# Kernel tuning notes

Hardware: AMD Instinct MI355X
Metric: run time of the kernel (lower is better)

Reference implementation:

```python
import jax, jax.numpy as jnp
import numpy as np

N_DETS = 50000
DEG = 32
N_EDGES = N_DETS * DEG

def _xavier(key, fan_in, fan_out):
    lim = np.sqrt(6.0 / (fan_in + fan_out)).astype(np.float32)
    return jax.random.uniform(key, (fan_in, fan_out), jnp.float32, -lim, lim)

def setup_inputs() -> dict:
    key = jax.random.key(0)
    ks = jax.random.split(key, 10)
    detFeatures = jax.random.normal(ks[0], (N_DETS, 128), jnp.float32)
    # every detection has exactly DEG neighbor pairs -> sorted segment ids, no empty segments
    cIdxs = jnp.repeat(jnp.arange(N_DETS, dtype=jnp.int64), DEG)
    nIdxs = jax.random.randint(ks[1], (N_EDGES,), 0, N_DETS, jnp.int64)
    pairFeatures = jax.random.normal(ks[2], (N_EDGES, 32), jnp.float32)
    return {
        "detFeatures": detFeatures,
        "cIdxs": cIdxs,
        "nIdxs": nIdxs,
        "pairFeatures": pairFeatures,
        "W_fc1": _xavier(ks[3], 128, 32), "b_fc1": jnp.zeros((32,), jnp.float32),
        "W_pw1": _xavier(ks[4], 96, 64), "b_pw1": jnp.zeros((64,), jnp.float32),
        "W_pw2": _xavier(ks[5], 64, 64), "b_pw2": jnp.zeros((64,), jnp.float32),
        "W_pm1": _xavier(ks[6], 64, 64), "b_pm1": jnp.zeros((64,), jnp.float32),
        "W_pm2": _xavier(ks[7], 64, 64), "b_pm2": jnp.zeros((64,), jnp.float32),
        "W_out": _xavier(ks[8], 64, 128), "b_out": jnp.zeros((128,), jnp.float32),
    }

def reference(detFeatures, cIdxs, nIdxs, pairFeatures,
              W_fc1, b_fc1, W_pw1, b_pw1, W_pw2, b_pw2,
              W_pm1, b_pm1, W_pm2, b_pm2, W_out, b_out):
    relu = jax.nn.relu
    # fc1: [N,128] -> [N,32]
    h = relu(detFeatures @ W_fc1 + b_fc1)
    # gather center / neighbor feats per pair; zero neighbor feats on identity rows
    cFeats = h[cIdxs]                                   # [E,32]
    nFeats = jnp.where((cIdxs == nIdxs)[:, None], 0.0, h[nIdxs])  # [E,32]
    x = jnp.concatenate((pairFeatures, cFeats, nFeats), axis=1)   # [E,96]
    x = relu(x @ W_pw1 + b_pw1)                         # [E,64]
    x = relu(x @ W_pw2 + b_pw2)                         # [E,64]
    # per-detection segment max (replaces the O(N) python loop)
    m = jax.ops.segment_max(x, cIdxs, num_segments=detFeatures.shape[0])  # [N,64]
    m = relu(m @ W_pm1 + b_pm1)
    m = relu(m @ W_pm2 + b_pm2)
    refined = m @ W_out + b_out                         # [N,128]
    return relu(detFeatures + refined)
```

## Files before the change

kernel.cpp:

```cpp
#include <hip/hip_runtime.h>

#define NDET 50000
#define DEG 32
#define NEDGE (NDET * DEG)
#define NGROUP (NEDGE / 64)

typedef __attribute__((ext_vector_type(8))) short short8;
typedef __attribute__((ext_vector_type(4))) float f32x4;

__device__ inline unsigned short f2bf(float x) {
    return (unsigned short)((__builtin_bit_cast(unsigned int, x) + 0x8000u) >> 16);
}

__device__ inline short8 pack8(f32x4 a, f32x4 b) {
    short8 r;
    r[0] = (short)f2bf(a[0]); r[1] = (short)f2bf(a[1]);
    r[2] = (short)f2bf(a[2]); r[3] = (short)f2bf(a[3]);
    r[4] = (short)f2bf(b[0]); r[5] = (short)f2bf(b[1]);
    r[6] = (short)f2bf(b[2]); r[7] = (short)f2bf(b[3]);
    return r;
}

__global__ __launch_bounds__(256, 4) void fc1_kernel(
    const float* __restrict__ detF,
    const float* __restrict__ W,
    const float* __restrict__ b,
    unsigned short* __restrict__ hbf)
{
    __shared__ __align__(16) unsigned short WT[32 * 136];

    const int tid  = threadIdx.x;
    const int lane = tid & 63;
    const int wv   = tid >> 6;
    const int m16  = lane & 15;
    const int q    = lane >> 4;

    for (int i = tid; i < 32 * 128; i += 256) {
        int n = i >> 7, k = i & 127;
        WT[n * 136 + k] = f2bf(W[k * 32 + n]);
    }
    __syncthreads();

    const int g = blockIdx.x * 4 + wv;
    if (g >= (NDET + 63) / 64) return;
    const int d0 = g * 64;

    f32x4 acc[4][2];
#pragma unroll
    for (int nt = 0; nt < 2; nt++) {
        float c0 = b[nt * 16 + m16];
#pragma unroll
        for (int mt = 0; mt < 4; mt++) acc[mt][nt] = (f32x4){c0, c0, c0, c0};
    }

#pragma unroll
    for (int ks = 0; ks < 4; ks++) {
#pragma unroll
        for (int mt = 0; mt < 4; mt++) {
            int row = d0 + mt * 16 + m16;
            if (row >= NDET) row = NDET - 1;
            const float* pr = detF + (size_t)row * 128 + ks * 32 + q * 8;
            short8 a = pack8(*(const f32x4*)pr, *(const f32x4*)(pr + 4));
#pragma unroll
            for (int nt = 0; nt < 2; nt++) {
                short8 bf = *(const short8*)&WT[(nt * 16 + m16) * 136 + ks * 32 + q * 8];
                acc[mt][nt] = __builtin_amdgcn_mfma_f32_16x16x32_bf16(a, bf, acc[mt][nt], 0, 0, 0);
            }
        }
    }

#pragma unroll
    for (int mt = 0; mt < 4; mt++)
#pragma unroll
        for (int r = 0; r < 4; r++) {
            int row = d0 + mt * 16 + q * 4 + r;
            if (row < NDET) {
#pragma unroll
                for (int nt = 0; nt < 2; nt++)
                    hbf[(size_t)row * 32 + nt * 16 + m16] = f2bf(fmaxf(acc[mt][nt][r], 0.0f));
            }
        }
}

__global__ __launch_bounds__(256, 3) void edge_kernel(
    const unsigned short* __restrict__ hbf,
    const int* __restrict__ nIdx,
    const float* __restrict__ pairF,
    const float* __restrict__ W1,
    const float* __restrict__ b1,
    const float* __restrict__ W2,
    const float* __restrict__ b2,
    unsigned short* __restrict__ m_bf)
{
    __shared__ __align__(16) unsigned short Y1s[4][64 * 72];
    __shared__ __align__(16) unsigned short W2T[64 * 72];

    const int tid  = threadIdx.x;
    const int lane = tid & 63;
    const int wv   = tid >> 6;
    const int m16  = lane & 15;
    const int q    = lane >> 4;

    unsigned short* st = &Y1s[0][0];
    for (int i = tid; i < 64 * 96; i += 256) {
        int n = i / 96, k = i - n * 96;
        st[i] = f2bf(W1[k * 64 + n]);
    }
    for (int i = tid; i < 64 * 64; i += 256) {
        int n = i >> 6, k = i & 63;
        W2T[n * 72 + k] = f2bf(W2[k * 64 + n]);
    }
    __syncthreads();

    short8 w1f[3][4];
#pragma unroll
    for (int nt = 0; nt < 4; nt++) {
        const unsigned short* base = &st[(nt * 16 + m16) * 96];
        w1f[0][nt] = *(const short8*)&base[q * 8];
        w1f[1][nt] = *(const short8*)&base[64 + q * 8];
        w1f[2][nt] = *(const short8*)&base[32 + q * 8];
    }
    float b1r[4], b2r[4];
#pragma unroll
    for (int nt = 0; nt < 4; nt++) {
        b1r[nt] = b1[nt * 16 + m16];
        b2r[nt] = b2[nt * 16 + m16];
    }
    __syncthreads();

    unsigned short* Y1w = &Y1s[wv][0];

    const int wstride = (int)gridDim.x * 4;
    int g = blockIdx.x * 4 + wv;
    if (g >= NGROUP) return;

    int    ni[4];
    f32x4  pv[4][2];
    short8 nb[4];
    short8 cf2[2];

#define PREF(gg)                                                                  \
    {                                                                             \
        const int E0p = (gg) * 64, d0p = (gg) * 2;                                \
        _Pragma("unroll")                                                         \
        for (int mt = 0; mt < 4; mt++) {                                          \
            int e = E0p + mt * 16 + m16;                                          \
            ni[mt] = __builtin_nontemporal_load(&nIdx[e]);                        \
            const float* pr = pairF + (size_t)e * 32 + q * 8;                     \
            pv[mt][0] = __builtin_nontemporal_load((const f32x4*)pr);             \
            pv[mt][1] = __builtin_nontemporal_load((const f32x4*)(pr + 4));       \
            nb[mt] = *(const short8*)&hbf[(size_t)ni[mt] * 32 + q * 8];           \
        }                                                                         \
        cf2[0] = *(const short8*)&hbf[(size_t)d0p * 32 + q * 8];                  \
        cf2[1] = *(const short8*)&hbf[(size_t)(d0p + 1) * 32 + q * 8];            \
    }

    PREF(g);
    const short8 zr = {0, 0, 0, 0, 0, 0, 0, 0};

    while (true) {
        const int d0 = g * 2;
        short8 ap[4], an[4], ac[4];
#pragma unroll
        for (int mt = 0; mt < 4; mt++) {
            ap[mt] = pack8(pv[mt][0], pv[mt][1]);
            an[mt] = (ni[mt] == d0 + (mt >> 1)) ? zr : nb[mt];
            ac[mt] = cf2[mt >> 1];
        }
        const int gn = g + wstride;
        const bool more = (gn < NGROUP);
        PREF(more ? gn : g);

        f32x4 acc[4][4];
#pragma unroll
        for (int mt = 0; mt < 4; mt++)
#pragma unroll
            for (int nt = 0; nt < 4; nt++) {
                float c0 = b1r[nt];
                acc[mt][nt] = (f32x4){c0, c0, c0, c0};
            }
#pragma unroll
        for (int mt = 0; mt < 4; mt++)
#pragma unroll
            for (int nt = 0; nt < 4; nt++) {
                acc[mt][nt] = __builtin_amdgcn_mfma_f32_16x16x32_bf16(ap[mt], w1f[0][nt], acc[mt][nt], 0, 0, 0);
                acc[mt][nt] = __builtin_amdgcn_mfma_f32_16x16x32_bf16(an[mt], w1f[1][nt], acc[mt][nt], 0, 0, 0);
                acc[mt][nt] = __builtin_amdgcn_mfma_f32_16x16x32_bf16(ac[mt], w1f[2][nt], acc[mt][nt], 0, 0, 0);
            }

#pragma unroll
        for (int mt = 0; mt < 4; mt++)
#pragma unroll
            for (int nt = 0; nt < 4; nt++)
#pragma unroll
                for (int r = 0; r < 4; r++)
                    Y1w[(mt * 16 + q * 4 + r) * 72 + nt * 16 + m16] =
                        f2bf(fmaxf(acc[mt][nt][r], 0.0f));

        f32x4 acc2[4][4];
#pragma unroll
        for (int mt = 0; mt < 4; mt++)
#pragma unroll
            for (int nt = 0; nt < 4; nt++) {
                float c0 = b2r[nt];
                acc2[mt][nt] = (f32x4){c0, c0, c0, c0};
            }
#pragma unroll
        for (int ks = 0; ks < 2; ks++) {
            short8 af[4];
#pragma unroll
            for (int mt = 0; mt < 4; mt++)
                af[mt] = *(const short8*)&Y1w[(mt * 16 + m16) * 72 + ks * 32 + q * 8];
#pragma unroll
            for (int nt = 0; nt < 4; nt++) {
                short8 wf = *(const short8*)&W2T[(nt * 16 + m16) * 72 + ks * 32 + q * 8];
#pragma unroll
                for (int mt = 0; mt < 4; mt++)
                    acc2[mt][nt] = __builtin_amdgcn_mfma_f32_16x16x32_bf16(af[mt], wf, acc2[mt][nt], 0, 0, 0);
            }
        }

#pragma unroll
        for (int d = 0; d < 2; d++)
#pragma unroll
            for (int nt = 0; nt < 4; nt++) {
                float v = 0.0f;
#pragma unroll
                for (int mt = 2 * d; mt < 2 * d + 2; mt++)
#pragma unroll
                    for (int r = 0; r < 4; r++) v = fmaxf(v, acc2[mt][nt][r]);
                v = fmaxf(v, __shfl_xor(v, 16));
                v = fmaxf(v, __shfl_xor(v, 32));
                if (q == 0) m_bf[(size_t)(d0 + d) * 64 + nt * 16 + m16] = f2bf(v);
            }

        if (!more) break;
        g = gn;
    }
#undef PREF
}

__global__ __launch_bounds__(256, 2) void tail_kernel(
    const float* __restrict__ detF,
    const unsigned short* __restrict__ m_bf,
    const float* __restrict__ Wm1, const float* __restrict__ bm1,
    const float* __restrict__ Wm2, const float* __restrict__ bm2,
    const float* __restrict__ Wo,  const float* __restrict__ bo,
    float* __restrict__ out)
{
    __shared__ __align__(16) unsigned short W1T[64 * 72];
    __shared__ __align__(16) unsigned short W2T[64 * 72];
    __shared__ __align__(16) unsigned short WoT[128 * 72];
    __shared__ __align__(16) unsigned short Tt[4][64 * 72];

    const int tid  = threadIdx.x;
    const int lane = tid & 63;
    const int wv   = tid >> 6;
    const int m16  = lane & 15;
    const int q    = lane >> 4;

    for (int i = tid; i < 64 * 64; i += 256) {
        int n = i >> 6, k = i & 63;
        W1T[n * 72 + k] = f2bf(Wm1[k * 64 + n]);
        W2T[n * 72 + k] = f2bf(Wm2[k * 64 + n]);
    }
    for (int i = tid; i < 128 * 64; i += 256) {
        int n = i >> 6, k = i & 63;
        WoT[n * 72 + k] = f2bf(Wo[k * 128 + n]);
    }
    __syncthreads();

    float bm1r[4], bm2r[4], bor[8];
#pragma unroll
    for (int nt = 0; nt < 4; nt++) {
        bm1r[nt] = bm1[nt * 16 + m16];
        bm2r[nt] = bm2[nt * 16 + m16];
    }
#pragma unroll
    for (int nt = 0; nt < 8; nt++) bor[nt] = bo[nt * 16 + m16];

    unsigned short* Tw = &Tt[wv][0];
    const int NTG = (NDET + 63) / 64;

    for (int gI = blockIdx.x * 4 + wv; gI < NTG; gI += (int)gridDim.x * 4) {
        const int d0 = gI * 64;

        f32x4 acc[4][4];
#pragma unroll
        for (int mt = 0; mt < 4; mt++)
#pragma unroll
            for (int nt = 0; nt < 4; nt++) {
                float c0 = bm1r[nt];
                acc[mt][nt] = (f32x4){c0, c0, c0, c0};
            }
#pragma unroll
        for (int ks = 0; ks < 2; ks++) {
            short8 af[4];
#pragma unroll
            for (int mt = 0; mt < 4; mt++) {
                int row = d0 + mt * 16 + m16;
                if (row >= NDET) row = NDET - 1;
                af[mt] = *(const short8*)&m_bf[(size_t)row * 64 + ks * 32 + q * 8];
            }
#pragma unroll
            for (int mt = 0; mt < 4; mt++)
#pragma unroll
                for (int nt = 0; nt < 4; nt++) {
                    short8 bf = *(const short8*)&W1T[(nt * 16 + m16) * 72 + ks * 32 + q * 8];
                    acc[mt][nt] = __builtin_amdgcn_mfma_f32_16x16x32_bf16(af[mt], bf, acc[mt][nt], 0, 0, 0);
                }
        }
#pragma unroll
        for (int mt = 0; mt < 4; mt++)
#pragma unroll
            for (int nt = 0; nt < 4; nt++)
#pragma unroll
                for (int r = 0; r < 4; r++)
                    Tw[(mt * 16 + q * 4 + r) * 72 + nt * 16 + m16] =
                        f2bf(fmaxf(acc[mt][nt][r], 0.0f));

#pragma unroll
        for (int mt = 0; mt < 4; mt++)
#pragma unroll
            for (int nt = 0; nt < 4; nt++) {
                float c0 = bm2r[nt];
                acc[mt][nt] = (f32x4){c0, c0, c0, c0};
            }
#pragma unroll
        for (int ks = 0; ks < 2; ks++) {
            short8 af[4];
#pragma unroll
            for (int mt = 0; mt < 4; mt++)
                af[mt] = *(const short8*)&Tw[(mt * 16 + m16) * 72 + ks * 32 + q * 8];
#pragma unroll
            for (int mt = 0; mt < 4; mt++)
#pragma unroll
                for (int nt = 0; nt < 4; nt++) {
                    short8 bf = *(const short8*)&W2T[(nt * 16 + m16) * 72 + ks * 32 + q * 8];
                    acc[mt][nt] = __builtin_amdgcn_mfma_f32_16x16x32_bf16(af[mt], bf, acc[mt][nt], 0, 0, 0);
                }
        }
#pragma unroll
        for (int mt = 0; mt < 4; mt++)
#pragma unroll
            for (int nt = 0; nt < 4; nt++)
#pragma unroll
                for (int r = 0; r < 4; r++)
                    Tw[(mt * 16 + q * 4 + r) * 72 + nt * 16 + m16] =
                        f2bf(fmaxf(acc[mt][nt][r], 0.0f));

        short8 a3[4][2];
#pragma unroll
        for (int ks = 0; ks < 2; ks++)
#pragma unroll
            for (int mt = 0; mt < 4; mt++)
                a3[mt][ks] = *(const short8*)&Tw[(mt * 16 + m16) * 72 + ks * 32 + q * 8];

#pragma unroll
        for (int h2 = 0; h2 < 2; h2++) {
            f32x4 acc3[4][4];
#pragma unroll
            for (int mt = 0; mt < 4; mt++)
#pragma unroll
                for (int nt = 0; nt < 4; nt++) {
                    float c0 = bor[h2 * 4 + nt];
                    acc3[mt][nt] = (f32x4){c0, c0, c0, c0};
                }
#pragma unroll
            for (int ks = 0; ks < 2; ks++)
#pragma unroll
                for (int mt = 0; mt < 4; mt++)
#pragma unroll
                    for (int nt = 0; nt < 4; nt++) {
                        short8 bf = *(const short8*)&WoT[((h2 * 4 + nt) * 16 + m16) * 72 + ks * 32 + q * 8];
                        acc3[mt][nt] = __builtin_amdgcn_mfma_f32_16x16x32_bf16(a3[mt][ks], bf, acc3[mt][nt], 0, 0, 0);
                    }
#pragma unroll
            for (int mt = 0; mt < 4; mt++)
#pragma unroll
                for (int r = 0; r < 4; r++) {
                    int row = d0 + mt * 16 + q * 4 + r;
                    if (row < NDET) {
#pragma unroll
                        for (int nt = 0; nt < 4; nt++) {
                            int col = (h2 * 4 + nt) * 16 + m16;
                            float v = detF[(size_t)row * 128 + col] + acc3[mt][nt][r];
                            out[(size_t)row * 128 + col] = fmaxf(v, 0.0f);
                        }
                    }
                }
        }
    }
}

extern "C" void kernel_launch(void* const* d_in, const int* in_sizes, int n_in,
                              void* d_out, int out_size, void* d_ws, size_t ws_size,
                              hipStream_t stream)
{
    const float* detF  = (const float*)d_in[0];
    const int*   nIdx  = (const int*)d_in[2];
    const float* pairF = (const float*)d_in[3];
    const float* W_fc1 = (const float*)d_in[4];
    const float* b_fc1 = (const float*)d_in[5];
    const float* W_pw1 = (const float*)d_in[6];
    const float* b_pw1 = (const float*)d_in[7];
    const float* W_pw2 = (const float*)d_in[8];
    const float* b_pw2 = (const float*)d_in[9];
    const float* W_pm1 = (const float*)d_in[10];
    const float* b_pm1 = (const float*)d_in[11];
    const float* W_pm2 = (const float*)d_in[12];
    const float* b_pm2 = (const float*)d_in[13];
    const float* W_out = (const float*)d_in[14];
    const float* b_out = (const float*)d_in[15];
    float* out = (float*)d_out;

    unsigned short* hbf  = (unsigned short*)d_ws;
    unsigned short* m_bf = hbf + (size_t)NDET * 32;

    fc1_kernel<<<(NDET + 255) / 256, 256, 0, stream>>>(detF, W_fc1, b_fc1, hbf);
    edge_kernel<<<768, 256, 0, stream>>>(hbf, nIdx, pairF,
                                         W_pw1, b_pw1, W_pw2, b_pw2, m_bf);
    tail_kernel<<<256, 256, 0, stream>>>(detF, m_bf, W_pm1, b_pm1, W_pm2, b_pm2,
                                         W_out, b_out, out);
}
```

Baseline: 462.2 us.

## Cut edge kernel register pressure to raise occupancy, restage prefetch pipeline

W1 fragments now stay in LDS and are reloaded per MFMA step instead of being held in registers. Each 64-edge group is processed in two 32-edge halves, which shrinks the accumulator arrays and the Y1 staging buffer. The prefetch becomes a deeper but lighter pipeline: neighbour indices are loaded two groups ahead, neighbour features one group ahead, and pair features in the current iteration. Launch bounds go to 4 waves and the grid to 1024 blocks to raise occupancy, at the cost of extra LDS reads and less latency hiding for the pairF loads.

```diff
diff --git a/kernel.cpp b/kernel.cpp
--- a/kernel.cpp
+++ b/kernel.cpp
@@ -82,7 +82,7 @@
         }
 }
 
-__global__ __launch_bounds__(256, 3) void edge_kernel(
+__global__ __launch_bounds__(256, 4) void edge_kernel(
     const unsigned short* __restrict__ hbf,
     const int* __restrict__ nIdx,
     const float* __restrict__ pairF,
@@ -92,8 +92,9 @@
     const float* __restrict__ b2,
     unsigned short* __restrict__ m_bf)
 {
-    __shared__ __align__(16) unsigned short Y1s[4][64 * 72];
+    __shared__ __align__(16) unsigned short W1T[64 * 104];
     __shared__ __align__(16) unsigned short W2T[64 * 72];
+    __shared__ __align__(16) unsigned short Y1s[4][32 * 72];
 
     const int tid  = threadIdx.x;
     const int lane = tid & 63;
@@ -101,10 +102,9 @@
     const int m16  = lane & 15;
     const int q    = lane >> 4;
 
-    unsigned short* st = &Y1s[0][0];
     for (int i = tid; i < 64 * 96; i += 256) {
         int n = i / 96, k = i - n * 96;
-        st[i] = f2bf(W1[k * 64 + n]);
+        W1T[n * 104 + k] = f2bf(W1[k * 64 + n]);
     }
     for (int i = tid; i < 64 * 64; i += 256) {
         int n = i >> 6, k = i & 63;
@@ -112,21 +112,12 @@
     }
     __syncthreads();
 
-    short8 w1f[3][4];
-#pragma unroll
-    for (int nt = 0; nt < 4; nt++) {
-        const unsigned short* base = &st[(nt * 16 + m16) * 96];
-        w1f[0][nt] = *(const short8*)&base[q * 8];
-        w1f[1][nt] = *(const short8*)&base[64 + q * 8];
-        w1f[2][nt] = *(const short8*)&base[32 + q * 8];
-    }
     float b1r[4], b2r[4];
 #pragma unroll
     for (int nt = 0; nt < 4; nt++) {
         b1r[nt] = b1[nt * 16 + m16];
         b2r[nt] = b2[nt * 16 + m16];
     }
-    __syncthreads();
 
     unsigned short* Y1w = &Y1s[wv][0];
 
@@ -134,110 +125,139 @@
     int g = blockIdx.x * 4 + wv;
     if (g >= NGROUP) return;
 
+    const short8 zr = {0, 0, 0, 0, 0, 0, 0, 0};
+
     int    ni[4];
-    f32x4  pv[4][2];
+    int    sk[4];
     short8 nb[4];
-    short8 cf2[2];
-
-#define PREF(gg)                                                                  \
-    {                                                                             \
-        const int E0p = (gg) * 64, d0p = (gg) * 2;                                \
-        _Pragma("unroll")                                                         \
-        for (int mt = 0; mt < 4; mt++) {                                          \
-            int e = E0p + mt * 16 + m16;                                          \
-            ni[mt] = __builtin_nontemporal_load(&nIdx[e]);                        \
-            const float* pr = pairF + (size_t)e * 32 + q * 8;                     \
-            pv[mt][0] = __builtin_nontemporal_load((const f32x4*)pr);             \
-            pv[mt][1] = __builtin_nontemporal_load((const f32x4*)(pr + 4));       \
-            nb[mt] = *(const short8*)&hbf[(size_t)ni[mt] * 32 + q * 8];           \
-        }                                                                         \
-        cf2[0] = *(const short8*)&hbf[(size_t)d0p * 32 + q * 8];                  \
-        cf2[1] = *(const short8*)&hbf[(size_t)(d0p + 1) * 32 + q * 8];            \
-    }
-
-    PREF(g);
-    const short8 zr = {0, 0, 0, 0, 0, 0, 0, 0};
+
+#pragma unroll
+    for (int mt = 0; mt < 4; mt++)
+        ni[mt] = __builtin_nontemporal_load(&nIdx[g * 64 + mt * 16 + m16]);
+#pragma unroll
+    for (int mt = 0; mt < 4; mt++) {
+        sk[mt] = (ni[mt] == g * 2 + (mt >> 1));
+        nb[mt] = *(const short8*)&hbf[(size_t)ni[mt] * 32 + q * 8];
+    }
+    {
+        int g1 = g + wstride;
+        int gl = (g1 < NGROUP) ? g1 : g;
+#pragma unroll
+        for (int mt = 0; mt < 4; mt++)
+            ni[mt] = __builtin_nontemporal_load(&nIdx[gl * 64 + mt * 16 + m16]);
+    }
 
     while (true) {
         const int d0 = g * 2;
-        short8 ap[4], an[4], ac[4];
+        const int gn = g + wstride;
+        const bool more = (gn < NGROUP);
+        const int gt = more ? gn : g;
+
+        f32x4 pv[4][2];
+#pragma unroll
+        for (int mt = 0; mt < 4; mt++) {
+            const float* pr = pairF + (size_t)(g * 64 + mt * 16 + m16) * 32 + q * 8;
+            pv[mt][0] = __builtin_nontemporal_load((const f32x4*)pr);
+            pv[mt][1] = __builtin_nontemporal_load((const f32x4*)(pr + 4));
+        }
+        short8 ac2[2];
+        ac2[0] = *(const short8*)&hbf[(size_t)d0 * 32 + q * 8];
+        ac2[1] = *(const short8*)&hbf[(size_t)(d0 + 1) * 32 + q * 8];
+
+        short8 ap[4], an[4];
 #pragma unroll
         for (int mt = 0; mt < 4; mt++) {
             ap[mt] = pack8(pv[mt][0], pv[mt][1]);
-            an[mt] = (ni[mt] == d0 + (mt >> 1)) ? zr : nb[mt];
-            ac[mt] = cf2[mt >> 1];
-        }
-        const int gn = g + wstride;
-        const bool more = (gn < NGROUP);
-        PREF(more ? gn : g);
-
-        f32x4 acc[4][4];
-#pragma unroll
-        for (int mt = 0; mt < 4; mt++)
+            an[mt] = sk[mt] ? zr : nb[mt];
+        }
+
+#pragma unroll
+        for (int mt = 0; mt < 4; mt++) {
+            int s = (ni[mt] == gt * 2 + (mt >> 1));
+            nb[mt] = *(const short8*)&hbf[(size_t)ni[mt] * 32 + q * 8];
+            sk[mt] = s;
+        }
+        {
+            const int gnn = gn + wstride;
+            const int gl2 = (more && gnn < NGROUP) ? gnn : gt;
+#pragma unroll
+            for (int mt = 0; mt < 4; mt++)
+                ni[mt] = __builtin_nontemporal_load(&nIdx[gl2 * 64 + mt * 16 + m16]);
+        }
+
+#pragma unroll
+        for (int h = 0; h < 2; h++) {
+            f32x4 acc[2][4];
+
+#pragma unroll
+            for (int j = 0; j < 2; j++)
+#pragma unroll
+                for (int nt = 0; nt < 4; nt++) {
+                    float c0 = b1r[nt];
+                    acc[j][nt] = (f32x4){c0, c0, c0, c0};
+                }
 #pragma unroll
             for (int nt = 0; nt < 4; nt++) {
-                float c0 = b1r[nt];
-                acc[mt][nt] = (f32x4){c0, c0, c0, c0};
-            }
-#pragma unroll
-        for (int mt = 0; mt < 4; mt++)
+                const unsigned short* wb = &W1T[(nt * 16 + m16) * 104 + q * 8];
+                short8 w0 = *(const short8*)&wb[0];
+                acc[0][nt] = __builtin_amdgcn_mfma_f32_16x16x32_bf16(ap[2 * h],     w0, acc[0][nt], 0, 0, 0);
+                acc[1][nt] = __builtin_amdgcn_mfma_f32_16x16x32_bf16(ap[2 * h + 1], w0, acc[1][nt], 0, 0, 0);
+                short8 w1 = *(const short8*)&wb[64];
+                acc[0][nt] = __builtin_amdgcn_mfma_f32_16x16x32_bf16(an[2 * h],     w1, acc[0][nt], 0, 0, 0);
+                acc[1][nt] = __builtin_amdgcn_mfma_f32_16x16x32_bf16(an[2 * h + 1], w1, acc[1][nt], 0, 0, 0);
+                short8 w2 = *(const short8*)&wb[32];
+                acc[0][nt] = __builtin_amdgcn_mfma_f32_16x16x32_bf16(ac2[h], w2, acc[0][nt], 0, 0, 0);
+                acc[1][nt] = __builtin_amdgcn_mfma_f32_16x16x32_bf16(ac2[h], w2, acc[1][nt], 0, 0, 0);
+            }
+
+#pragma unroll
+            for (int j = 0; j < 2; j++)
+#pragma unroll
+                for (int nt = 0; nt < 4; nt++)
+#pragma unroll
+                    for (int r = 0; r < 4; r++)
+                        Y1w[(j * 16 + q * 4 + r) * 72 + nt * 16 + m16] =
+                            f2bf(fmaxf(acc[j][nt][r], 0.0f));
+
+            short8 af0[2], af1[2];
+#pragma unroll
+            for (int j = 0; j < 2; j++) {
+                af0[j] = *(const short8*)&Y1w[(j * 16 + m16) * 72 + q * 8];
+                af1[j] = *(const short8*)&Y1w[(j * 16 + m16) * 72 + 32 + q * 8];
+            }
+#pragma unroll
+            for (int j = 0; j < 2; j++)
+#pragma unroll
+                for (int nt = 0; nt < 4; nt++) {
+                    float c0 = b2r[nt];
+                    acc[j][nt] = (f32x4){c0, c0, c0, c0};
+                }
 #pragma unroll
             for (int nt = 0; nt < 4; nt++) {
-                acc[mt][nt] = __builtin_amdgcn_mfma_f32_16x16x32_bf16(ap[mt], w1f[0][nt], acc[mt][nt], 0, 0, 0);
-                acc[mt][nt] = __builtin_amdgcn_mfma_f32_16x16x32_bf16(an[mt], w1f[1][nt], acc[mt][nt], 0, 0, 0);
-                acc[mt][nt] = __builtin_amdgcn_mfma_f32_16x16x32_bf16(ac[mt], w1f[2][nt], acc[mt][nt], 0, 0, 0);
-            }
-
-#pragma unroll
-        for (int mt = 0; mt < 4; mt++)
-#pragma unroll
-            for (int nt = 0; nt < 4; nt++)
-#pragma unroll
-                for (int r = 0; r < 4; r++)
-                    Y1w[(mt * 16 + q * 4 + r) * 72 + nt * 16 + m16] =
-                        f2bf(fmaxf(acc[mt][nt][r], 0.0f));
-
-        f32x4 acc2[4][4];
-#pragma unroll
-        for (int mt = 0; mt < 4; mt++)
-#pragma unroll
-            for (int nt = 0; nt < 4; nt++) {
-                float c0 = b2r[nt];
-                acc2[mt][nt] = (f32x4){c0, c0, c0, c0};
-            }
-#pragma unroll
-        for (int ks = 0; ks < 2; ks++) {
-            short8 af[4];
-#pragma unroll
-            for (int mt = 0; mt < 4; mt++)
-                af[mt] = *(const short8*)&Y1w[(mt * 16 + m16) * 72 + ks * 32 + q * 8];
-#pragma unroll
-            for (int nt = 0; nt < 4; nt++) {
-                short8 wf = *(const short8*)&W2T[(nt * 16 + m16) * 72 + ks * 32 + q * 8];
-#pragma unroll
-                for (int mt = 0; mt < 4; mt++)
-                    acc2[mt][nt] = __builtin_amdgcn_mfma_f32_16x16x32_bf16(af[mt], wf, acc2[mt][nt], 0, 0, 0);
-            }
-        }
-
-#pragma unroll
-        for (int d = 0; d < 2; d++)
+                short8 wf = *(const short8*)&W2T[(nt * 16 + m16) * 72 + q * 8];
+                acc[0][nt] = __builtin_amdgcn_mfma_f32_16x16x32_bf16(af0[0], wf, acc[0][nt], 0, 0, 0);
+                acc[1][nt] = __builtin_amdgcn_mfma_f32_16x16x32_bf16(af0[1], wf, acc[1][nt], 0, 0, 0);
+                wf = *(const short8*)&W2T[(nt * 16 + m16) * 72 + 32 + q * 8];
+                acc[0][nt] = __builtin_amdgcn_mfma_f32_16x16x32_bf16(af1[0], wf, acc[0][nt], 0, 0, 0);
+                acc[1][nt] = __builtin_amdgcn_mfma_f32_16x16x32_bf16(af1[1], wf, acc[1][nt], 0, 0, 0);
+            }
+
 #pragma unroll
             for (int nt = 0; nt < 4; nt++) {
                 float v = 0.0f;
 #pragma unroll
-                for (int mt = 2 * d; mt < 2 * d + 2; mt++)
-#pragma unroll
-                    for (int r = 0; r < 4; r++) v = fmaxf(v, acc2[mt][nt][r]);
+                for (int j = 0; j < 2; j++)
+#pragma unroll
+                    for (int r = 0; r < 4; r++) v = fmaxf(v, acc[j][nt][r]);
                 v = fmaxf(v, __shfl_xor(v, 16));
                 v = fmaxf(v, __shfl_xor(v, 32));
-                if (q == 0) m_bf[(size_t)(d0 + d) * 64 + nt * 16 + m16] = f2bf(v);
-            }
+                if (q == 0) m_bf[(size_t)(d0 + h) * 64 + nt * 16 + m16] = f2bf(v);
+            }
+        }
 
         if (!more) break;
         g = gn;
     }
-#undef PREF
 }
 
 __global__ __launch_bounds__(256, 2) void tail_kernel(
@@ -418,8 +438,8 @@
     unsigned short* m_bf = hbf + (size_t)NDET * 32;
 
     fc1_kernel<<<(NDET + 255) / 256, 256, 0, stream>>>(detF, W_fc1, b_fc1, hbf);
-    edge_kernel<<<768, 256, 0, stream>>>(hbf, nIdx, pairF,
-                                         W_pw1, b_pw1, W_pw2, b_pw2, m_bf);
+    edge_kernel<<<1024, 256, 0, stream>>>(hbf, nIdx, pairF,
+                                          W_pw1, b_pw1, W_pw2, b_pw2, m_bf);
     tail_kernel<<<256, 256, 0, stream>>>(detF, m_bf, W_pm1, b_pm1, W_pm2, b_pm2,
                                          W_out, b_out, out);
 }
```

Result: faster. 416.0 us (-10.0%).
